# Optimization experiments

Measured on AMD Instinct MI355X. Metric: run time of the kernel, lower is better.

## Reference

```python
import jax, jax.numpy as jnp
import numpy as np

N_HEAD = 16


def setup_inputs() -> dict:
    key = jax.random.key(0)
    ks = jax.random.split(key, 5)
    B, T, C = 4, 2048, 1024
    s = 1.0 / np.sqrt(C)
    x = jax.random.normal(ks[0], (B, T, C), dtype=jnp.float32)
    wq = jax.random.normal(ks[1], (C, C), dtype=jnp.float32) * s
    wk = jax.random.normal(ks[2], (C, C), dtype=jnp.float32) * s
    wv = jax.random.normal(ks[3], (C, C), dtype=jnp.float32) * s
    wo = jax.random.normal(ks[4], (C, C), dtype=jnp.float32) * s
    return {"x": x, "wq": wq, "wk": wk, "wv": wv, "wo": wo}


def _attn(x, wq, wk, wv, wo):
    B, T, C = x.shape
    H = N_HEAD
    D = C // H
    scale = 1.0 / np.sqrt(D)
    # nn.Linear(x) = x @ W.T; weights stored as [out, in]
    q = (x @ wq.T).reshape(B, T, H, D).transpose(0, 2, 1, 3)  # [B,H,T,D]
    k = (x @ wk.T).reshape(B, T, H, D).transpose(0, 2, 1, 3)
    v = (x @ wv.T).reshape(B, T, H, D).transpose(0, 2, 1, 3)
    scores = jnp.einsum("bhtd,bhsd->bhts", q, k) * scale  # [B,H,T,T]
    mask = jnp.triu(jnp.full((T, T), -jnp.inf, dtype=scores.dtype), k=1)
    attn = jax.nn.softmax(scores + mask, axis=-1)
    out = jnp.einsum("bhts,bhsd->bhtd", attn, v)  # [B,H,T,D]
    out = out.transpose(0, 2, 1, 3).reshape(B, T, C)
    return out @ wo.T


def reference(x, wq, wk, wv, wo):
    return _attn(x, wq, wk, wv, wo)
```

## Files before the change

kernel.cpp:

```cpp
#include <hip/hip_runtime.h>

typedef __bf16 bf16x8 __attribute__((ext_vector_type(8)));
typedef float f32x4 __attribute__((ext_vector_type(4)));
typedef unsigned short ushortx8 __attribute__((ext_vector_type(8)));
typedef unsigned short ushortx4 __attribute__((ext_vector_type(4)));

#if __has_builtin(__builtin_amdgcn_exp2f)
#define EXP2F(x) __builtin_amdgcn_exp2f(x)
#else
#define EXP2F(x) exp2f(x)
#endif
#if __has_builtin(__builtin_amdgcn_rcpf)
#define RCPF(x) __builtin_amdgcn_rcpf(x)
#else
#define RCPF(x) (1.0f / (x))
#endif

__device__ __forceinline__ unsigned short f2bf(float f) {
    unsigned int u = __builtin_bit_cast(unsigned int, f);
    u += 0x7fffu + ((u >> 16) & 1u);
    return (unsigned short)(u >> 16);
}

__device__ __forceinline__ bf16x8 ld_frag(const unsigned short* p) {
    return __builtin_bit_cast(bf16x8, *(const ushortx8*)p);
}

__device__ __forceinline__ unsigned int pack_bf2(float lo, float hi) {
#if __has_builtin(__builtin_amdgcn_cvt_pk_bf16_f32)
    typedef __bf16 bf16x2 __attribute__((ext_vector_type(2)));
    bf16x2 v = __builtin_amdgcn_cvt_pk_bf16_f32(lo, hi);
    return __builtin_bit_cast(unsigned int, v);
#else
    unsigned int ulo = __builtin_bit_cast(unsigned int, lo) + 0x8000u;
    unsigned int uhi = __builtin_bit_cast(unsigned int, hi) + 0x8000u;
    return __builtin_amdgcn_perm(uhi, ulo, 0x07060302u);
#endif
}

__device__ __forceinline__ void async_cp16(const unsigned short* g, unsigned short* l) {
    __builtin_amdgcn_global_load_lds(
        (const __attribute__((address_space(1))) unsigned int*)g,
        (__attribute__((address_space(3))) unsigned int*)(unsigned long)(unsigned long long)(uintptr_t)
            reinterpret_cast<uintptr_t>(l),
        16, 0, 0);
}

__global__ void cvt_kernel(const float* __restrict__ src, unsigned short* __restrict__ dst, int n4) {
    int i = blockIdx.x * blockDim.x + threadIdx.x;
    if (i < n4) {
        float4 f = ((const float4*)src)[i];
        ushortx4 u = { f2bf(f.x), f2bf(f.y), f2bf(f.z), f2bf(f.w) };
        ((ushortx4*)dst)[i] = u;
    }
}

__global__ void cvt4_kernel(const float* __restrict__ s0, const float* __restrict__ s1,
                            const float* __restrict__ s2, const float* __restrict__ s3,
                            unsigned short* __restrict__ dst) {
    const float* src = (blockIdx.y == 0) ? s0 : (blockIdx.y == 1) ? s1 : (blockIdx.y == 2) ? s2 : s3;
    unsigned short* d = dst + (size_t)blockIdx.y * (1024 * 1024);
    int i = blockIdx.x * blockDim.x + threadIdx.x;
    float4 f = ((const float4*)src)[i];
    ushortx4 u = { f2bf(f.x), f2bf(f.y), f2bf(f.z), f2bf(f.w) };
    ((ushortx4*)d)[i] = u;
}

__global__ __launch_bounds__(256, 2) void qkv_gemm(
    const unsigned short* __restrict__ xb,
    const unsigned short* __restrict__ wqb,
    const unsigned short* __restrict__ wkb,
    const unsigned short* __restrict__ wvb,
    unsigned short* __restrict__ q_ws,
    unsigned short* __restrict__ k_ws,
    unsigned short* __restrict__ v_ws)
{
    __shared__ __align__(16) unsigned short A_lds[128 * 32];
    __shared__ __align__(16) unsigned short B_lds[128 * 32];

    const int tid = threadIdx.x;
    const int wv = tid >> 6;
    const int lane = tid & 63;
    const int quad = lane >> 4;
    const int l15 = lane & 15;
    const int wm = wv >> 1;
    const int wn = wv & 1;

    const int m0 = blockIdx.x * 128;
    const int mat = blockIdx.y >> 3;
    const int n0 = (blockIdx.y & 7) * 128;
    const unsigned short* wb = (mat == 0) ? wqb : (mat == 1 ? wkb : wvb);

    const int srow = lane >> 2;
    const int scol = (lane & 3) * 8;
    const unsigned short* ag0 = xb + (size_t)(m0 + wv * 32 + srow) * 1024 + scol;
    const unsigned short* ag1 = ag0 + 16 * 1024;
    const unsigned short* bg0 = wb + (size_t)(n0 + wv * 32 + srow) * 1024 + scol;
    const unsigned short* bg1 = bg0 + 16 * 1024;
    unsigned short* la0 = A_lds + (wv * 32) * 32;
    unsigned short* la1 = A_lds + (wv * 32 + 16) * 32;
    unsigned short* lb0 = B_lds + (wv * 32) * 32;
    unsigned short* lb1 = B_lds + (wv * 32 + 16) * 32;

    f32x4 acc[4][4] = {};

    for (int kt = 0; kt < 1024; kt += 32) {
        __syncthreads();
        async_cp16(ag0 + kt, la0);
        async_cp16(ag1 + kt, la1);
        async_cp16(bg0 + kt, lb0);
        async_cp16(bg1 + kt, lb1);
        __builtin_amdgcn_s_waitcnt(0x0F70);
        __syncthreads();

        bf16x8 af[4], bf[4];
#pragma unroll
        for (int i = 0; i < 4; ++i)
            af[i] = ld_frag(A_lds + (wm * 64 + i * 16 + l15) * 32 + quad * 8);
#pragma unroll
        for (int i = 0; i < 4; ++i)
            bf[i] = ld_frag(B_lds + (wn * 64 + i * 16 + l15) * 32 + quad * 8);
#pragma unroll
        for (int i = 0; i < 4; ++i)
#pragma unroll
            for (int j = 0; j < 4; ++j)
                acc[i][j] = __builtin_amdgcn_mfma_f32_16x16x32_bf16(af[i], bf[j], acc[i][j], 0, 0, 0);
    }

    const float qscale = 0.125f * 1.4426950408889634f;
    const int mbase = m0 + wm * 64;
    const int nbase = n0 + wn * 64;
#pragma unroll
    for (int i = 0; i < 4; ++i) {
        const int mrow = mbase + i * 16 + quad * 4;
        const int b = mrow >> 11;
        const int trow = mrow & 2047;
#pragma unroll
        for (int j = 0; j < 4; ++j) {
            const int nloc = nbase + j * 16 + l15;
            const int h = nloc >> 6, d = nloc & 63;
            if (mat == 2) {
                ushortx4 pk = { f2bf(acc[i][j][0]), f2bf(acc[i][j][1]),
                                f2bf(acc[i][j][2]), f2bf(acc[i][j][3]) };
                *(ushortx4*)&v_ws[(((size_t)(b * 16 + h)) * 64 + d) * 2048 + trow] = pk;
            } else {
                unsigned short* dst = (mat == 0) ? q_ws : k_ws;
                float sc = (mat == 0) ? qscale : 1.0f;
                size_t base = (((size_t)(b * 16 + h)) * 2048 + trow) * 64 + d;
                dst[base]       = f2bf(acc[i][j][0] * sc);
                dst[base + 64]  = f2bf(acc[i][j][1] * sc);
                dst[base + 128] = f2bf(acc[i][j][2] * sc);
                dst[base + 192] = f2bf(acc[i][j][3] * sc);
            }
        }
    }
}

__global__ __launch_bounds__(256, 2) void attn_kernel(
    const unsigned short* __restrict__ q_ws,
    const unsigned short* __restrict__ k_ws,
    const unsigned short* __restrict__ v_ws,
    unsigned short* __restrict__ o_ws)
{
    __shared__ __align__(16) unsigned short K_lds[128][72];
    __shared__ __align__(16) unsigned short Vt_lds[64][136];
    __shared__ __align__(16) unsigned short P_lds[128][136];

    const int tid = threadIdx.x;
    const int wvid = tid >> 6, lane = tid & 63, quad = lane >> 4, l15 = lane & 15;
    const int bh = blockIdx.x;
    const int b = bh >> 4, h = bh & 15;
    const int bt = 15 - (int)blockIdx.y;
    const int t0 = bt * 128;

    const unsigned short* qb = q_ws + (size_t)bh * 2048 * 64;
    const unsigned short* kb = k_ws + (size_t)bh * 2048 * 64;
    const unsigned short* vb = v_ws + (size_t)bh * 64 * 2048;

    ushortx8 ones_u = { 0x3F80, 0x3F80, 0x3F80, 0x3F80, 0x3F80, 0x3F80, 0x3F80, 0x3F80 };
    const bf16x8 ones = __builtin_bit_cast(bf16x8, ones_u);

    bf16x8 bq[2][2];
#pragma unroll
    for (int it = 0; it < 2; ++it)
#pragma unroll
        for (int kk = 0; kk < 2; ++kk)
            bq[it][kk] = ld_frag(qb + (size_t)(t0 + wvid * 32 + it * 16 + l15) * 64 + kk * 32 + quad * 8);

    f32x4 acc_o[2][4] = {};
    f32x4 l_acc[2] = {};

    const int kr = tid >> 1, kc = (tid & 1) * 32;
    const int vr = tid >> 2, vc = (tid & 3) * 32;

    for (int j = 0; j <= bt; ++j) {
        const int s0 = j * 128;
        ushortx8 kvr[4], vvr[4];
#pragma unroll
        for (int u = 0; u < 4; ++u)
            kvr[u] = *(const ushortx8*)(kb + (size_t)(s0 + kr) * 64 + kc + u * 8);
#pragma unroll
        for (int u = 0; u < 4; ++u)
            vvr[u] = *(const ushortx8*)(vb + (size_t)vr * 2048 + s0 + vc + u * 8);
        __syncthreads();
#pragma unroll
        for (int u = 0; u < 4; ++u) *(ushortx8*)&K_lds[kr][kc + u * 8] = kvr[u];
#pragma unroll
        for (int u = 0; u < 4; ++u) *(ushortx8*)&Vt_lds[vr][vc + u * 8] = vvr[u];
        __syncthreads();

        f32x4 sacc[2][8] = {};
#pragma unroll
        for (int is = 0; is < 8; ++is) {
            bf16x8 k0 = ld_frag(&K_lds[is * 16 + l15][quad * 8]);
            bf16x8 k1 = ld_frag(&K_lds[is * 16 + l15][32 + quad * 8]);
            sacc[0][is] = __builtin_amdgcn_mfma_f32_16x16x32_bf16(k0, bq[0][0], sacc[0][is], 0, 0, 0);
            sacc[0][is] = __builtin_amdgcn_mfma_f32_16x16x32_bf16(k1, bq[0][1], sacc[0][is], 0, 0, 0);
            sacc[1][is] = __builtin_amdgcn_mfma_f32_16x16x32_bf16(k0, bq[1][0], sacc[1][is], 0, 0, 0);
            sacc[1][is] = __builtin_amdgcn_mfma_f32_16x16x32_bf16(k1, bq[1][1], sacc[1][is], 0, 0, 0);
        }

        if (j == bt) {
#pragma unroll
            for (int it = 0; it < 2; ++it) {
                const int tl = wvid * 32 + it * 16 + l15;
#pragma unroll
                for (int is = 0; is < 8; ++is)
#pragma unroll
                    for (int r = 0; r < 4; ++r) {
                        const int sl = is * 16 + quad * 4 + r;
                        if (sl > tl) sacc[it][is][r] = -1.0e30f;
                    }
            }
        }

#pragma unroll
        for (int it = 0; it < 2; ++it) {
            const int row = wvid * 32 + it * 16 + l15;
#pragma unroll
            for (int is = 0; is < 8; ++is) {
                float p0 = EXP2F(sacc[it][is][0]);
                float p1 = EXP2F(sacc[it][is][1]);
                float p2 = EXP2F(sacc[it][is][2]);
                float p3 = EXP2F(sacc[it][is][3]);
                uint2 pk = { pack_bf2(p0, p1), pack_bf2(p2, p3) };
                *(uint2*)&P_lds[row][is * 16 + quad * 4] = pk;
            }
        }

        __threadfence_block();

#pragma unroll
        for (int kk = 0; kk < 4; ++kk) {
            bf16x8 p0 = ld_frag(&P_lds[wvid * 32 + l15][kk * 32 + quad * 8]);
            bf16x8 p1 = ld_frag(&P_lds[wvid * 32 + 16 + l15][kk * 32 + quad * 8]);
            l_acc[0] = __builtin_amdgcn_mfma_f32_16x16x32_bf16(p0, ones, l_acc[0], 0, 0, 0);
            l_acc[1] = __builtin_amdgcn_mfma_f32_16x16x32_bf16(p1, ones, l_acc[1], 0, 0, 0);
#pragma unroll
            for (int id = 0; id < 4; ++id) {
                bf16x8 bv = ld_frag(&Vt_lds[id * 16 + l15][kk * 32 + quad * 8]);
                acc_o[0][id] = __builtin_amdgcn_mfma_f32_16x16x32_bf16(p0, bv, acc_o[0][id], 0, 0, 0);
                acc_o[1][id] = __builtin_amdgcn_mfma_f32_16x16x32_bf16(p1, bv, acc_o[1][id], 0, 0, 0);
            }
        }
    }

#pragma unroll
    for (int it = 0; it < 2; ++it) {
        f32x4 rinv;
#pragma unroll
        for (int r = 0; r < 4; ++r) rinv[r] = RCPF(l_acc[it][r]);
#pragma unroll
        for (int id = 0; id < 4; ++id)
#pragma unroll
            for (int r = 0; r < 4; ++r) {
                int tg = t0 + wvid * 32 + it * 16 + quad * 4 + r;
                int c = h * 64 + id * 16 + l15;
                o_ws[(size_t)(b * 2048 + tg) * 1024 + c] = f2bf(acc_o[it][id][r] * rinv[r]);
            }
    }
}

__global__ __launch_bounds__(256, 2) void out_gemm(
    const unsigned short* __restrict__ ob,
    const unsigned short* __restrict__ wob,
    float* __restrict__ out)
{
    __shared__ __align__(16) unsigned short A_lds[128 * 32];
    __shared__ __align__(16) unsigned short B_lds[128 * 32];

    const int tid = threadIdx.x;
    const int wv = tid >> 6;
    const int lane = tid & 63;
    const int quad = lane >> 4;
    const int l15 = lane & 15;
    const int wm = wv >> 1;
    const int wn = wv & 1;

    const int m0 = blockIdx.x * 128;
    const int n0 = blockIdx.y * 128;

    const int srow = lane >> 2;
    const int scol = (lane & 3) * 8;
    const unsigned short* ag0 = ob + (size_t)(m0 + wv * 32 + srow) * 1024 + scol;
    const unsigned short* ag1 = ag0 + 16 * 1024;
    const unsigned short* bg0 = wob + (size_t)(n0 + wv * 32 + srow) * 1024 + scol;
    const unsigned short* bg1 = bg0 + 16 * 1024;
    unsigned short* la0 = A_lds + (wv * 32) * 32;
    unsigned short* la1 = A_lds + (wv * 32 + 16) * 32;
    unsigned short* lb0 = B_lds + (wv * 32) * 32;
    unsigned short* lb1 = B_lds + (wv * 32 + 16) * 32;

    f32x4 acc[4][4] = {};

    for (int kt = 0; kt < 1024; kt += 32) {
        __syncthreads();
        async_cp16(ag0 + kt, la0);
        async_cp16(ag1 + kt, la1);
        async_cp16(bg0 + kt, lb0);
        async_cp16(bg1 + kt, lb1);
        __builtin_amdgcn_s_waitcnt(0x0F70);
        __syncthreads();

        bf16x8 af[4], bf[4];
#pragma unroll
        for (int i = 0; i < 4; ++i)
            af[i] = ld_frag(A_lds + (wm * 64 + i * 16 + l15) * 32 + quad * 8);
#pragma unroll
        for (int i = 0; i < 4; ++i)
            bf[i] = ld_frag(B_lds + (wn * 64 + i * 16 + l15) * 32 + quad * 8);
#pragma unroll
        for (int i = 0; i < 4; ++i)
#pragma unroll
            for (int j = 0; j < 4; ++j)
                acc[i][j] = __builtin_amdgcn_mfma_f32_16x16x32_bf16(af[i], bf[j], acc[i][j], 0, 0, 0);
    }

    const int mbase = m0 + wm * 64;
    const int nbase = n0 + wn * 64;
#pragma unroll
    for (int i = 0; i < 4; ++i) {
        const int mrow = mbase + i * 16 + quad * 4;
#pragma unroll
        for (int j = 0; j < 4; ++j) {
            const int ncol = nbase + j * 16 + l15;
            float* dst = out + (size_t)mrow * 1024 + ncol;
            dst[0]        = acc[i][j][0];
            dst[1024]     = acc[i][j][1];
            dst[2048]     = acc[i][j][2];
            dst[3072]     = acc[i][j][3];
        }
    }
}

extern "C" void kernel_launch(void* const* d_in, const int* in_sizes, int n_in,
                              void* d_out, int out_size, void* d_ws, size_t ws_size,
                              hipStream_t stream) {
    const float* x  = (const float*)d_in[0];
    const float* wq = (const float*)d_in[1];
    const float* wk = (const float*)d_in[2];
    const float* wv = (const float*)d_in[3];
    const float* wo = (const float*)d_in[4];
    float* out = (float*)d_out;

    unsigned short* ws = (unsigned short*)d_ws;
    unsigned short* xb   = ws;
    unsigned short* wqb  = xb  + (size_t)8192 * 1024;
    unsigned short* wkb  = wqb + (size_t)1024 * 1024;
    unsigned short* wvb  = wkb + (size_t)1024 * 1024;
    unsigned short* wob  = wvb + (size_t)1024 * 1024;
    unsigned short* q_ws = wob + (size_t)1024 * 1024;
    unsigned short* k_ws = q_ws + (size_t)8192 * 1024;
    unsigned short* v_ws = k_ws + (size_t)8192 * 1024;
    unsigned short* o_ws = v_ws + (size_t)8192 * 1024;

    int n4 = (8192 * 1024) / 4;
    cvt_kernel<<<(n4 + 255) / 256, 256, 0, stream>>>(x, xb, n4);
    cvt4_kernel<<<dim3(1024, 4), 256, 0, stream>>>(wq, wk, wv, wo, wqb);

    qkv_gemm<<<dim3(64, 24), 256, 0, stream>>>(xb, wqb, wkb, wvb, q_ws, k_ws, v_ws);
    attn_kernel<<<dim3(64, 16), 256, 0, stream>>>(q_ws, k_ws, v_ws, o_ws);
    out_gemm<<<dim3(64, 8), 256, 0, stream>>>(o_ws, wob, out);
}
```

Measured before the change: 237.3 us.

## Load K/V fragments directly from global into registers, swizzle P in LDS

The attention kernel drops the K and V LDS staging and both __syncthreads per tile. Each wave now loads its K and V MFMA fragments straight from global memory into registers, and prefetches the next K tile during the current PV step. The P buffer is flattened with an XOR swizzle to avoid LDS bank conflicts, and s_setprio wraps the MFMA blocks. Each wave now makes redundant global loads (through L2/L1) instead of sharing them via LDS, and register pressure rises, which may hurt occupancy.

Measured after the change: 318.7 us. 1.34x slower.

```diff
diff --git a/kernel.cpp b/kernel.cpp
--- a/kernel.cpp
+++ b/kernel.cpp
@@ -162,9 +162,7 @@
     const unsigned short* __restrict__ v_ws,
     unsigned short* __restrict__ o_ws)
 {
-    __shared__ __align__(16) unsigned short K_lds[128][72];
-    __shared__ __align__(16) unsigned short Vt_lds[64][136];
-    __shared__ __align__(16) unsigned short P_lds[128][136];
+    __shared__ __align__(16) unsigned short P_lds[128 * 128];
 
     const int tid = threadIdx.x;
     const int wvid = tid >> 6, lane = tid & 63, quad = lane >> 4, l15 = lane & 15;
@@ -190,35 +188,32 @@
     f32x4 acc_o[2][4] = {};
     f32x4 l_acc[2] = {};
 
-    const int kr = tid >> 1, kc = (tid & 1) * 32;
-    const int vr = tid >> 2, vc = (tid & 3) * 32;
+    const int sw = (l15 & 7) << 4;
+    char* const pb = (char*)P_lds;
+    char* const prow0 = pb + (wvid * 32 + l15) * 256;
+    char* const prow1 = pb + (wvid * 32 + 16 + l15) * 256;
+
+    bf16x8 kf[8][2];
+#pragma unroll
+    for (int is = 0; is < 8; ++is) {
+        const unsigned short* kr = kb + (size_t)(is * 16 + l15) * 64 + quad * 8;
+        kf[is][0] = ld_frag(kr);
+        kf[is][1] = ld_frag(kr + 32);
+    }
 
     for (int j = 0; j <= bt; ++j) {
         const int s0 = j * 128;
-        ushortx8 kvr[4], vvr[4];
-#pragma unroll
-        for (int u = 0; u < 4; ++u)
-            kvr[u] = *(const ushortx8*)(kb + (size_t)(s0 + kr) * 64 + kc + u * 8);
-#pragma unroll
-        for (int u = 0; u < 4; ++u)
-            vvr[u] = *(const ushortx8*)(vb + (size_t)vr * 2048 + s0 + vc + u * 8);
-        __syncthreads();
-#pragma unroll
-        for (int u = 0; u < 4; ++u) *(ushortx8*)&K_lds[kr][kc + u * 8] = kvr[u];
-#pragma unroll
-        for (int u = 0; u < 4; ++u) *(ushortx8*)&Vt_lds[vr][vc + u * 8] = vvr[u];
-        __syncthreads();
 
         f32x4 sacc[2][8] = {};
+        __builtin_amdgcn_s_setprio(1);
 #pragma unroll
         for (int is = 0; is < 8; ++is) {
-            bf16x8 k0 = ld_frag(&K_lds[is * 16 + l15][quad * 8]);
-            bf16x8 k1 = ld_frag(&K_lds[is * 16 + l15][32 + quad * 8]);
-            sacc[0][is] = __builtin_amdgcn_mfma_f32_16x16x32_bf16(k0, bq[0][0], sacc[0][is], 0, 0, 0);
-            sacc[0][is] = __builtin_amdgcn_mfma_f32_16x16x32_bf16(k1, bq[0][1], sacc[0][is], 0, 0, 0);
-            sacc[1][is] = __builtin_amdgcn_mfma_f32_16x16x32_bf16(k0, bq[1][0], sacc[1][is], 0, 0, 0);
-            sacc[1][is] = __builtin_amdgcn_mfma_f32_16x16x32_bf16(k1, bq[1][1], sacc[1][is], 0, 0, 0);
-        }
+            sacc[0][is] = __builtin_amdgcn_mfma_f32_16x16x32_bf16(kf[is][0], bq[0][0], sacc[0][is], 0, 0, 0);
+            sacc[0][is] = __builtin_amdgcn_mfma_f32_16x16x32_bf16(kf[is][1], bq[0][1], sacc[0][is], 0, 0, 0);
+            sacc[1][is] = __builtin_amdgcn_mfma_f32_16x16x32_bf16(kf[is][0], bq[1][0], sacc[1][is], 0, 0, 0);
+            sacc[1][is] = __builtin_amdgcn_mfma_f32_16x16x32_bf16(kf[is][1], bq[1][1], sacc[1][is], 0, 0, 0);
+        }
+        __builtin_amdgcn_s_setprio(0);
 
         if (j == bt) {
 #pragma unroll
@@ -236,7 +231,7 @@
 
 #pragma unroll
         for (int it = 0; it < 2; ++it) {
-            const int row = wvid * 32 + it * 16 + l15;
+            char* prow = pb + (wvid * 32 + it * 16 + l15) * 256;
 #pragma unroll
             for (int is = 0; is < 8; ++is) {
                 float p0 = EXP2F(sacc[it][is][0]);
@@ -244,24 +239,47 @@
                 float p2 = EXP2F(sacc[it][is][2]);
                 float p3 = EXP2F(sacc[it][is][3]);
                 uint2 pk = { pack_bf2(p0, p1), pack_bf2(p2, p3) };
-                *(uint2*)&P_lds[row][is * 16 + quad * 4] = pk;
-            }
-        }
-
-        __threadfence_block();
+                *(uint2*)(prow + ((is * 32 + quad * 8) ^ sw)) = pk;
+            }
+        }
+
+        bf16x8 vf[4][4];
+#pragma unroll
+        for (int kk = 0; kk < 2; ++kk)
+#pragma unroll
+            for (int id = 0; id < 4; ++id)
+                vf[kk][id] = ld_frag(vb + (size_t)(id * 16 + l15) * 2048 + s0 + kk * 32 + quad * 8);
+        if (j < bt) {
+            const int s1 = s0 + 128;
+#pragma unroll
+            for (int is = 0; is < 8; ++is) {
+                const unsigned short* kr = kb + (size_t)(s1 + is * 16 + l15) * 64 + quad * 8;
+                kf[is][0] = ld_frag(kr);
+                kf[is][1] = ld_frag(kr + 32);
+            }
+        }
+
+        asm volatile("s_waitcnt lgkmcnt(0)" ::: "memory");
+        __builtin_amdgcn_sched_barrier(0);
 
 #pragma unroll
         for (int kk = 0; kk < 4; ++kk) {
-            bf16x8 p0 = ld_frag(&P_lds[wvid * 32 + l15][kk * 32 + quad * 8]);
-            bf16x8 p1 = ld_frag(&P_lds[wvid * 32 + 16 + l15][kk * 32 + quad * 8]);
+            bf16x8 p0 = ld_frag((const unsigned short*)(prow0 + ((kk * 64 + quad * 16) ^ sw)));
+            bf16x8 p1 = ld_frag((const unsigned short*)(prow1 + ((kk * 64 + quad * 16) ^ sw)));
+            if (kk < 2) {
+#pragma unroll
+                for (int id = 0; id < 4; ++id)
+                    vf[kk + 2][id] = ld_frag(vb + (size_t)(id * 16 + l15) * 2048 + s0 + (kk + 2) * 32 + quad * 8);
+            }
+            __builtin_amdgcn_s_setprio(1);
             l_acc[0] = __builtin_amdgcn_mfma_f32_16x16x32_bf16(p0, ones, l_acc[0], 0, 0, 0);
             l_acc[1] = __builtin_amdgcn_mfma_f32_16x16x32_bf16(p1, ones, l_acc[1], 0, 0, 0);
 #pragma unroll
             for (int id = 0; id < 4; ++id) {
-                bf16x8 bv = ld_frag(&Vt_lds[id * 16 + l15][kk * 32 + quad * 8]);
-                acc_o[0][id] = __builtin_amdgcn_mfma_f32_16x16x32_bf16(p0, bv, acc_o[0][id], 0, 0, 0);
-                acc_o[1][id] = __builtin_amdgcn_mfma_f32_16x16x32_bf16(p1, bv, acc_o[1][id], 0, 0, 0);
-            }
+                acc_o[0][id] = __builtin_amdgcn_mfma_f32_16x16x32_bf16(p0, vf[kk][id], acc_o[0][id], 0, 0, 0);
+                acc_o[1][id] = __builtin_amdgcn_mfma_f32_16x16x32_bf16(p1, vf[kk][id], acc_o[1][id], 0, 0, 0);
+            }
+            __builtin_amdgcn_s_setprio(0);
         }
     }
 
```
